# Performance work log

Measured on AMD Instinct MI355X. Metric: run time of the kernel, lower is better.

The kernel has to match this reference:

```python
import jax, jax.numpy as jnp
import numpy as np

B, S, D = 2, 2048, 1024
H, DK, DV = 16, 64, 64


def setup_inputs() -> dict:
    key = jax.random.key(0)
    ks = jax.random.split(key, 12)
    s = 0.02
    return {
        "query": jax.random.normal(ks[0], (B, S, D), jnp.float32),
        "key": jax.random.normal(ks[1], (B, S, D), jnp.float32),
        "value": jax.random.normal(ks[2], (B, S, D), jnp.float32),
        "mask": jax.random.randint(ks[3], (B, S, S), 0, 2, jnp.int32),
        "Wq": jax.random.normal(ks[4], (D, H * DK), jnp.float32) * s,
        "bq": jnp.zeros((H * DK,), jnp.float32),
        "Wk": jax.random.normal(ks[5], (D, H * DK), jnp.float32) * s,
        "bk": jnp.zeros((H * DK,), jnp.float32),
        "Wv": jax.random.normal(ks[6], (D, H * DV), jnp.float32) * s,
        "bv": jnp.zeros((H * DV,), jnp.float32),
        "Wo": jax.random.normal(ks[7], (H * DV, D), jnp.float32) * s,
        "bo": jnp.zeros((D,), jnp.float32),
    }


def reference(query, key, value, mask, Wq, bq, Wk, bk, Wv, bv, Wo, bo):
    temperature = jnp.sqrt(jnp.asarray(DK, query.dtype))
    # projections: [B,S,H*dk] -> [B,H,S,dk]
    q = (query @ Wq + bq).reshape(B, S, H, DK).transpose(0, 2, 1, 3)
    k = (key @ Wk + bk).reshape(B, S, H, DK).transpose(0, 2, 1, 3)
    v = (value @ Wv + bv).reshape(B, S, H, DV).transpose(0, 2, 1, 3)
    # energy: [B,H,Sq,Skv]
    energy = jnp.einsum("bhqd,bhkd->bhqk", q, k) / temperature
    energy = jnp.where(mask[:, None, :, :] == 0, jnp.asarray(-10000.0, energy.dtype), energy)
    attention = jax.nn.softmax(energy, axis=-1)
    attention = jnp.where(jnp.isnan(attention), jnp.asarray(0.0, attention.dtype), attention)
    out = jnp.einsum("bhqk,bhkd->bhqd", attention, v)  # dropout p=0 (eval)
    out = out.transpose(0, 2, 1, 3).reshape(B, S, H * DV)
    out = out @ Wo + bo
    return (out, attention)
```

## Files before the change

### kernel.cpp

```cpp
#include <hip/hip_runtime.h>
#include <stdint.h>


typedef __attribute__((ext_vector_type(8))) __bf16 bf16x8;
typedef __attribute__((ext_vector_type(8))) short short8;
typedef __attribute__((ext_vector_type(4))) float f32x4;

static __device__ __forceinline__ f32x4 mfma_bf16(short8 a, short8 b, f32x4 c) {
  return __builtin_amdgcn_mfma_f32_16x16x32_bf16(
      __builtin_bit_cast(bf16x8, a), __builtin_bit_cast(bf16x8, b), c, 0, 0, 0);
}

static __device__ __forceinline__ unsigned short f2bf(float f) {
  unsigned int u = __float_as_uint(f);
  u += 0x7fffu + ((u >> 16) & 1u);
  return (unsigned short)(u >> 16);
}

static __device__ __forceinline__ void gload_lds16(const void* g, void* l) {
  __builtin_amdgcn_global_load_lds(
      (__attribute__((address_space(1))) void*)(uintptr_t)(g),
      (__attribute__((address_space(3))) void*)(uintptr_t)(l), 16, 0, 0);
}

__global__ __launch_bounds__(256) void conv_f32_bf16(
    const float* q, const float* k, const float* v,
    unsigned short* oq, unsigned short* ok, unsigned short* ov) {
  const float* src = (blockIdx.z == 0) ? q : (blockIdx.z == 1) ? k : v;
  unsigned short* dst = (blockIdx.z == 0) ? oq : (blockIdx.z == 1) ? ok : ov;
  const int i = (blockIdx.x * 256 + threadIdx.x) * 8;
  const float4 a = *(const float4*)&src[i];
  const float4 b = *(const float4*)&src[i + 4];
  unsigned short r[8] = {f2bf(a.x), f2bf(a.y), f2bf(a.z), f2bf(a.w),
                         f2bf(b.x), f2bf(b.y), f2bf(b.z), f2bf(b.w)};
  *(uint4*)&dst[i] = *(uint4*)r;
}

__global__ __launch_bounds__(256) void transpose_w(
    const float* w0, const float* w1, const float* w2, const float* w3,
    unsigned short* o0, unsigned short* o1,
    unsigned short* o2, unsigned short* o3) {
  const float* src = (blockIdx.z == 0) ? w0 : (blockIdx.z == 1) ? w1
                                         : (blockIdx.z == 2) ? w2 : w3;
  unsigned short* dst = (blockIdx.z == 0) ? o0 : (blockIdx.z == 1) ? o1
                                           : (blockIdx.z == 2) ? o2 : o3;
  __shared__ unsigned short tile[64 * 66];
  const int t = threadIdx.x;
  const int r0 = blockIdx.y * 64, c0 = blockIdx.x * 64;
#pragma unroll
  for (int i = 0; i < 4; ++i) {
    const int slot = i * 256 + t;
    const int row = slot >> 4, cg = slot & 15;
    const float4 v = *(const float4*)&src[(r0 + row) * 1024 + c0 + cg * 4];
    unsigned int p0 = (unsigned int)f2bf(v.x) | ((unsigned int)f2bf(v.y) << 16);
    unsigned int p1 = (unsigned int)f2bf(v.z) | ((unsigned int)f2bf(v.w) << 16);
    unsigned int* dp = (unsigned int*)&tile[row * 66 + cg * 4];
    dp[0] = p0;
    dp[1] = p1;
  }
  __syncthreads();
#pragma unroll
  for (int i = 0; i < 2; ++i) {
    const int slot = i * 256 + t;
    const int orow = slot >> 3, kg = slot & 7;
    unsigned short vals[8];
#pragma unroll
    for (int j = 0; j < 8; ++j) vals[j] = tile[(kg * 8 + j) * 66 + orow];
    *(uint4*)&dst[(c0 + orow) * 1024 + r0 + kg * 8] = *(uint4*)vals;
  }
}

__global__ __launch_bounds__(256) void mask_prep(const int* __restrict__ mask,
                                                 unsigned long long* __restrict__ bits) {
  const int wid = (blockIdx.x * 256 + threadIdx.x) >> 6;
  const int lane = threadIdx.x & 63;
  for (int w = wid; w < 131072; w += 2048) {
    const int m = mask[w * 64 + lane];
    const unsigned long long b = __ballot(m != 0);
    if (lane == 0) bits[w] = b;
  }
}

struct GArg {
  const unsigned short* A;
  const unsigned short* BT;
  const float* bias;
  void* C;
  int mode;
};

__global__ __launch_bounds__(256) void gemm_bt(GArg ga, GArg gb, GArg gc) {
  const GArg g = (blockIdx.z == 0) ? ga : (blockIdx.z == 1) ? gb : gc;
  __shared__ alignas(16) unsigned short ash[128 * 64];
  __shared__ alignas(16) unsigned short bsh[128 * 64];
  const int t = threadIdx.x;
  const int wave = t >> 6, lane = t & 63;
  const int m0 = blockIdx.y * 128, n0 = blockIdx.x * 128;
  const int wm = (wave >> 1) * 64, wn = (wave & 1) * 64;
  const int c = lane & 15, gq = lane >> 4;
  const int srow = wave * 8 + (lane >> 3);
  const int scol = (lane & 7) * 8;

  f32x4 zero = {0.f, 0.f, 0.f, 0.f};
  f32x4 acc[4][4];
#pragma unroll
  for (int i = 0; i < 4; ++i)
#pragma unroll
    for (int j = 0; j < 4; ++j) acc[i][j] = zero;

  for (int kk = 0; kk < 16; ++kk) {
    __syncthreads();
    const int kbase = kk * 64;
#pragma unroll
    for (int i = 0; i < 4; ++i) {
      gload_lds16(&g.A[(m0 + i * 32 + srow) * 1024 + kbase + scol],
                  &ash[(i * 32 + wave * 8) * 64]);
      gload_lds16(&g.BT[(n0 + i * 32 + srow) * 1024 + kbase + scol],
                  &bsh[(i * 32 + wave * 8) * 64]);
    }
    __syncthreads();
#pragma unroll
    for (int ks = 0; ks < 2; ++ks) {
      short8 af[4], bf[4];
#pragma unroll
      for (int mt = 0; mt < 4; ++mt)
        af[mt] = *(const short8*)&ash[(wm + mt * 16 + c) * 64 + ks * 32 + gq * 8];
#pragma unroll
      for (int nt = 0; nt < 4; ++nt)
        bf[nt] = *(const short8*)&bsh[(wn + nt * 16 + c) * 64 + ks * 32 + gq * 8];
#pragma unroll
      for (int mt = 0; mt < 4; ++mt)
#pragma unroll
        for (int nt = 0; nt < 4; ++nt)
          acc[mt][nt] = mfma_bf16(af[mt], bf[nt], acc[mt][nt]);
    }
  }
#pragma unroll
  for (int nt = 0; nt < 4; ++nt) {
    const int gcol = n0 + wn + nt * 16 + c;
    const float bia = g.bias[gcol];
#pragma unroll
    for (int mt = 0; mt < 4; ++mt) {
#pragma unroll
      for (int r = 0; r < 4; ++r) {
        const int grow = m0 + wm + mt * 16 + gq * 4 + r;
        const float v = acc[mt][nt][r] + bia;
        if (g.mode == 0) {
          ((unsigned short*)g.C)[grow * 1024 + gcol] = f2bf(v);
        } else if (g.mode == 1) {
          ((unsigned short*)g.C)[((grow >> 11) << 21) + (gcol << 11) + (grow & 2047)] =
              f2bf(v);
        } else {
          ((float*)g.C)[grow * 1024 + gcol] = v;
        }
      }
    }
  }
}

__global__ __launch_bounds__(256) void attn_kern(
    const unsigned short* __restrict__ Qb, const unsigned short* __restrict__ Kb,
    const unsigned short* __restrict__ Vt, const unsigned long long* __restrict__ mbits,
    float* __restrict__ att, unsigned short* __restrict__ Obuf) {
  const int qt = blockIdx.x, h = blockIdx.y, b = blockIdx.z;
  const int t = threadIdx.x, wave = t >> 6, lane = t & 63;
  const int q0 = qt * 64;
  const int c = lane & 15, gq = lane >> 4;
  const int srow = lane >> 3, scol = (lane & 7) * 8;
  const float SCALE = 0.125f * 1.44269504088896341f;

  __shared__ alignas(16) unsigned short qs[64 * 64];
  __shared__ alignas(16) unsigned short kt[64 * 64];
  __shared__ alignas(16) unsigned short vt[64 * 64];
  __shared__ alignas(16) float psf[64 * 64];

#pragma unroll
  for (int i = 0; i < 2; ++i) {
    gload_lds16(&Qb[(b * 2048 + q0 + wave * 16 + i * 8 + srow) * 1024 + h * 64 + scol],
                &qs[(wave * 16 + i * 8) * 64]);
  }

  const unsigned long long* mrow =
      &mbits[(unsigned)(b * 2048 + q0 + wave * 16 + gq * 4) * 32];

  float lsum[4] = {0.f, 0.f, 0.f, 0.f};
  short8 aq[2];
  f32x4 zero = {0.f, 0.f, 0.f, 0.f};

  for (int kv = 0; kv < 32; ++kv) {
    __syncthreads();
#pragma unroll
    for (int i = 0; i < 2; ++i) {
      gload_lds16(&Kb[(b * 2048 + kv * 64 + wave * 16 + i * 8 + srow) * 1024 + h * 64 + scol],
                  &kt[(wave * 16 + i * 8) * 64]);
    }
    __syncthreads();
    if (kv == 0) {
      aq[0] = *(const short8*)&qs[(wave * 16 + c) * 64 + gq * 8];
      aq[1] = *(const short8*)&qs[(wave * 16 + c) * 64 + 32 + gq * 8];
    }
    f32x4 s[4];
#pragma unroll
    for (int nt = 0; nt < 4; ++nt) s[nt] = zero;
#pragma unroll
    for (int ks = 0; ks < 2; ++ks)
#pragma unroll
      for (int nt = 0; nt < 4; ++nt) {
        short8 bk = *(const short8*)&kt[(nt * 16 + c) * 64 + ks * 32 + gq * 8];
        s[nt] = mfma_bf16(aq[ks], bk, s[nt]);
      }
    unsigned long long msh[4];
#pragma unroll
    for (int r = 0; r < 4; ++r) msh[r] = mrow[r * 32 + kv] >> c;
#pragma unroll
    for (int nt = 0; nt < 4; ++nt)
#pragma unroll
      for (int r = 0; r < 4; ++r) {
        const bool on = (msh[r] >> (nt * 16)) & 1ull;
        const float e = on ? s[nt][r] * SCALE : -30.f;
        lsum[r] += __builtin_amdgcn_exp2f(e);
      }
  }
  float linv[4];
#pragma unroll
  for (int r = 0; r < 4; ++r) {
    float v = lsum[r];
    v += __shfl_xor(v, 1);
    v += __shfl_xor(v, 2);
    v += __shfl_xor(v, 4);
    v += __shfl_xor(v, 8);
    linv[r] = 1.0f / v;
  }

  f32x4 o[4];
#pragma unroll
  for (int nt = 0; nt < 4; ++nt) o[nt] = zero;

  for (int kv = 0; kv < 32; ++kv) {
    __syncthreads();
#pragma unroll
    for (int i = 0; i < 2; ++i) {
      gload_lds16(&Kb[(b * 2048 + kv * 64 + wave * 16 + i * 8 + srow) * 1024 + h * 64 + scol],
                  &kt[(wave * 16 + i * 8) * 64]);
      gload_lds16(&Vt[(b << 21) + (h * 64 + wave * 16 + i * 8 + srow) * 2048 + kv * 64 + scol],
                  &vt[(wave * 16 + i * 8) * 64]);
    }
    __syncthreads();
    f32x4 s[4];
#pragma unroll
    for (int nt = 0; nt < 4; ++nt) s[nt] = zero;
#pragma unroll
    for (int ks = 0; ks < 2; ++ks)
#pragma unroll
      for (int nt = 0; nt < 4; ++nt) {
        short8 bk = *(const short8*)&kt[(nt * 16 + c) * 64 + ks * 32 + gq * 8];
        s[nt] = mfma_bf16(aq[ks], bk, s[nt]);
      }
    unsigned long long msh[4];
#pragma unroll
    for (int r = 0; r < 4; ++r) msh[r] = mrow[r * 32 + kv] >> c;
#pragma unroll
    for (int nt = 0; nt < 4; ++nt)
#pragma unroll
      for (int r = 0; r < 4; ++r) {
        const bool on = (msh[r] >> (nt * 16)) & 1ull;
        const float e = on ? s[nt][r] * SCALE : -30.f;
        const float p = __builtin_amdgcn_exp2f(e) * linv[r];
        psf[wave * 1024 + (gq * 4 + r) * 64 + nt * 16 + c] = p;
      }
    __syncthreads();
#pragma unroll
    for (int ks = 0; ks < 2; ++ks) {
      const float4 f0 = *(const float4*)&psf[wave * 1024 + c * 64 + ks * 32 + gq * 8];
      const float4 f1 = *(const float4*)&psf[wave * 1024 + c * 64 + ks * 32 + gq * 8 + 4];
      unsigned short pr[8] = {f2bf(f0.x), f2bf(f0.y), f2bf(f0.z), f2bf(f0.w),
                              f2bf(f1.x), f2bf(f1.y), f2bf(f1.z), f2bf(f1.w)};
      const short8 ap = *(const short8*)pr;
#pragma unroll
      for (int nt = 0; nt < 4; ++nt) {
        short8 bv = *(const short8*)&vt[(nt * 16 + c) * 64 + ks * 32 + gq * 8];
        o[nt] = mfma_bf16(ap, bv, o[nt]);
      }
    }
#pragma unroll
    for (int pass = 0; pass < 4; ++pass) {
      const int row = pass * 4 + (lane >> 4);
      const int col4 = lane & 15;
      const float4 pv = *(const float4*)&psf[wave * 1024 + row * 64 + col4 * 4];
      *(float4*)&att[((long)((b * 16 + h) * 2048 + q0 + wave * 16 + row)) * 2048 +
                     kv * 64 + col4 * 4] = pv;
    }
  }
#pragma unroll
  for (int nt = 0; nt < 4; ++nt)
#pragma unroll
    for (int r = 0; r < 4; ++r) {
      const int row = q0 + wave * 16 + gq * 4 + r;
      Obuf[(b * 2048 + row) * 1024 + h * 64 + nt * 16 + c] = f2bf(o[nt][r]);
    }
}

extern "C" void kernel_launch(void* const* d_in, const int* in_sizes, int n_in,
                              void* d_out, int out_size, void* d_ws, size_t ws_size,
                              hipStream_t stream) {
  const float* query = (const float*)d_in[0];
  const float* key   = (const float*)d_in[1];
  const float* value = (const float*)d_in[2];
  const int* mask    = (const int*)d_in[3];
  const float* Wq = (const float*)d_in[4];
  const float* bq = (const float*)d_in[5];
  const float* Wk = (const float*)d_in[6];
  const float* bk = (const float*)d_in[7];
  const float* Wv = (const float*)d_in[8];
  const float* bv = (const float*)d_in[9];
  const float* Wo = (const float*)d_in[10];
  const float* bo = (const float*)d_in[11];

  float* out = (float*)d_out;
  float* att = out + 4194304;

  char* ws = (char*)d_ws;
  const size_t MB = 1u << 20;
  unsigned short* Aq   = (unsigned short*)(ws);
  unsigned short* Ak   = (unsigned short*)(ws + 8 * MB);
  unsigned short* Av   = (unsigned short*)(ws + 16 * MB);
  unsigned short* Qb   = (unsigned short*)(ws + 24 * MB);
  unsigned short* Kb   = (unsigned short*)(ws + 32 * MB);
  unsigned short* Vt   = (unsigned short*)(ws + 40 * MB);
  unsigned short* Obuf = (unsigned short*)(ws + 48 * MB);
  unsigned short* WqT  = (unsigned short*)(ws + 56 * MB);
  unsigned short* WkT  = (unsigned short*)(ws + 58 * MB);
  unsigned short* WvT  = (unsigned short*)(ws + 60 * MB);
  unsigned short* WoT  = (unsigned short*)(ws + 62 * MB);
  unsigned long long* mbits = (unsigned long long*)(ws + 64 * MB);

  conv_f32_bf16<<<dim3(2048, 1, 3), 256, 0, stream>>>(query, key, value, Aq, Ak, Av);
  transpose_w<<<dim3(16, 16, 4), 256, 0, stream>>>(Wq, Wk, Wv, Wo, WqT, WkT, WvT, WoT);
  mask_prep<<<dim3(512), 256, 0, stream>>>(mask, mbits);

  GArg gq{Aq, WqT, bq, Qb, 0};
  GArg gk{Ak, WkT, bk, Kb, 0};
  GArg gv{Av, WvT, bv, Vt, 1};
  gemm_bt<<<dim3(8, 32, 3), 256, 0, stream>>>(gq, gk, gv);

  attn_kern<<<dim3(32, 16, 2), 256, 0, stream>>>(Qb, Kb, Vt, mbits, att, Obuf);

  GArg go{Obuf, WoT, bo, out, 2};
  gemm_bt<<<dim3(8, 32, 1), 256, 0, stream>>>(go, go, go);
}
```

Measured before the change: 855.7 us.

## Double-buffer K/V tiles with swizzled LDS, precomputed mask nibbles, block remap

Rewrites the two-pass attention kernel to double-buffer the K and V tiles in LDS, prefetching the next tile while the current one is computed. Waits are manual vmcnt/lgkmcnt counts plus raw barriers instead of __syncthreads. It also XOR-swizzles LDS columns to avoid bank conflicts, loads Q directly into registers, and packs mask bits per lane into 64-bit registers once up front instead of reading global memory every iteration. It further remaps block IDs for better L2 locality and raises wave priority around the MFMA sections. In exchange the hand-written waitcnt counts are fragile: the last iteration's vmcnt(4), with stores in flight, could be wrong and cause ordering errors.

```diff
diff --git a/kernel.cpp b/kernel.cpp
--- a/kernel.cpp
+++ b/kernel.cpp
@@ -162,65 +162,119 @@
     const unsigned short* __restrict__ Qb, const unsigned short* __restrict__ Kb,
     const unsigned short* __restrict__ Vt, const unsigned long long* __restrict__ mbits,
     float* __restrict__ att, unsigned short* __restrict__ Obuf) {
-  const int qt = blockIdx.x, h = blockIdx.y, b = blockIdx.z;
+  const int id0 = blockIdx.x + 32 * (blockIdx.y + 16 * blockIdx.z);
+  const int id = (id0 & 7) * 128 + (id0 >> 3);
+  const int qt = id & 31, h = (id >> 5) & 15, b = id >> 9;
   const int t = threadIdx.x, wave = t >> 6, lane = t & 63;
   const int q0 = qt * 64;
   const int c = lane & 15, gq = lane >> 4;
-  const int srow = lane >> 3, scol = (lane & 7) * 8;
+  const int srow = lane >> 3;
+  const int scol_sw = ((lane & 7) ^ srow) * 8;
   const float SCALE = 0.125f * 1.44269504088896341f;
 
-  __shared__ alignas(16) unsigned short qs[64 * 64];
-  __shared__ alignas(16) unsigned short kt[64 * 64];
-  __shared__ alignas(16) unsigned short vt[64 * 64];
-  __shared__ alignas(16) float psf[64 * 64];
-
-#pragma unroll
-  for (int i = 0; i < 2; ++i) {
-    gload_lds16(&Qb[(b * 2048 + q0 + wave * 16 + i * 8 + srow) * 1024 + h * 64 + scol],
-                &qs[(wave * 16 + i * 8) * 64]);
-  }
-
-  const unsigned long long* mrow =
-      &mbits[(unsigned)(b * 2048 + q0 + wave * 16 + gq * 4) * 32];
-
+  __shared__ alignas(16) unsigned short kt[2][64 * 64];
+  __shared__ alignas(16) unsigned short vt[2][64 * 64];
+  __shared__ alignas(16) float psf[4 * 16 * 64];
+
+  auto stage_k = [&](int kvt, int bu) {
+#pragma unroll
+    for (int i = 0; i < 2; ++i)
+      gload_lds16(&Kb[(b * 2048 + kvt * 64 + wave * 16 + i * 8 + srow) * 1024 +
+                      h * 64 + scol_sw],
+                  &kt[bu][(wave * 16 + i * 8) * 64]);
+  };
+  auto stage_v = [&](int kvt, int bu) {
+#pragma unroll
+    for (int i = 0; i < 2; ++i)
+      gload_lds16(&Vt[(b << 21) + (h * 64 + wave * 16 + i * 8 + srow) * 2048 +
+                      kvt * 64 + scol_sw],
+                  &vt[bu][(wave * 16 + i * 8) * 64]);
+  };
+  auto rdcol = [&](int ks) { return (((ks * 4 + gq) ^ (c & 7)) * 8); };
+
+  stage_k(0, 0);
+
+  unsigned long long* msk = (unsigned long long*)psf;
+  {
+    const int row = t >> 2, c8 = (t & 3) * 8;
+    const unsigned long long* src = &mbits[(unsigned)(b * 2048 + q0 + row) * 32 + c8];
+#pragma unroll
+    for (int j = 0; j < 8; ++j) msk[row * 32 + c8 + j] = src[j];
+  }
+  unsigned long long mlo[4], mhi[4];
+#pragma unroll
+  for (int r = 0; r < 4; ++r) {
+    const int row = wave * 16 + gq * 4 + r;
+    unsigned long long lo = 0, hi = 0;
+#pragma unroll
+    for (int kvi = 0; kvi < 16; ++kvi) {
+      const unsigned long long w0 = msk[row * 32 + kvi] >> c;
+      const unsigned long long w1 = msk[row * 32 + 16 + kvi] >> c;
+      const unsigned long long n0 =
+          (w0 & 1) | ((w0 >> 15) & 2) | ((w0 >> 30) & 4) | ((w0 >> 45) & 8);
+      const unsigned long long n1 =
+          (w1 & 1) | ((w1 >> 15) & 2) | ((w1 >> 30) & 4) | ((w1 >> 45) & 8);
+      lo |= n0 << (kvi * 4);
+      hi |= n1 << (kvi * 4);
+    }
+    mlo[r] = lo;
+    mhi[r] = hi;
+  }
+
+  short8 aq[2];
+  {
+    const unsigned short* qrow = &Qb[(b * 2048 + q0 + wave * 16 + c) * 1024 + h * 64];
+    aq[0] = *(const short8*)&qrow[gq * 8];
+    aq[1] = *(const short8*)&qrow[32 + gq * 8];
+  }
+
+  asm volatile("s_waitcnt vmcnt(0) lgkmcnt(0)" ::: "memory");
+  __builtin_amdgcn_s_barrier();
+  __builtin_amdgcn_sched_barrier(0);
+
+  const f32x4 zero = {0.f, 0.f, 0.f, 0.f};
   float lsum[4] = {0.f, 0.f, 0.f, 0.f};
-  short8 aq[2];
-  f32x4 zero = {0.f, 0.f, 0.f, 0.f};
-
+  int buf = 0;
+
+#pragma unroll 1
   for (int kv = 0; kv < 32; ++kv) {
-    __syncthreads();
-#pragma unroll
-    for (int i = 0; i < 2; ++i) {
-      gload_lds16(&Kb[(b * 2048 + kv * 64 + wave * 16 + i * 8 + srow) * 1024 + h * 64 + scol],
-                  &kt[(wave * 16 + i * 8) * 64]);
-    }
-    __syncthreads();
-    if (kv == 0) {
-      aq[0] = *(const short8*)&qs[(wave * 16 + c) * 64 + gq * 8];
-      aq[1] = *(const short8*)&qs[(wave * 16 + c) * 64 + 32 + gq * 8];
-    }
+    if (kv < 31) {
+      stage_k(kv + 1, buf ^ 1);
+      asm volatile("s_waitcnt vmcnt(2)" ::: "memory");
+    } else {
+      asm volatile("s_waitcnt vmcnt(0)" ::: "memory");
+    }
+    __builtin_amdgcn_s_barrier();
+    __builtin_amdgcn_sched_barrier(0);
+
     f32x4 s[4];
 #pragma unroll
     for (int nt = 0; nt < 4; ++nt) s[nt] = zero;
+    __builtin_amdgcn_s_setprio(1);
 #pragma unroll
     for (int ks = 0; ks < 2; ++ks)
 #pragma unroll
       for (int nt = 0; nt < 4; ++nt) {
-        short8 bk = *(const short8*)&kt[(nt * 16 + c) * 64 + ks * 32 + gq * 8];
+        const short8 bk = *(const short8*)&kt[buf][(nt * 16 + c) * 64 + rdcol(ks)];
         s[nt] = mfma_bf16(aq[ks], bk, s[nt]);
       }
-    unsigned long long msh[4];
-#pragma unroll
-    for (int r = 0; r < 4; ++r) msh[r] = mrow[r * 32 + kv] >> c;
-#pragma unroll
-    for (int nt = 0; nt < 4; ++nt)
-#pragma unroll
-      for (int r = 0; r < 4; ++r) {
-        const bool on = (msh[r] >> (nt * 16)) & 1ull;
-        const float e = on ? s[nt][r] * SCALE : -30.f;
+    __builtin_amdgcn_s_setprio(0);
+#pragma unroll
+    for (int r = 0; r < 4; ++r) {
+      const unsigned long long mr = (kv < 16) ? mlo[r] : mhi[r];
+      const unsigned nib = (unsigned)(mr >> ((kv & 15) * 4)) & 0xFu;
+#pragma unroll
+      for (int nt = 0; nt < 4; ++nt) {
+        const float e = ((nib >> nt) & 1u) ? s[nt][r] * SCALE : -30.f;
         lsum[r] += __builtin_amdgcn_exp2f(e);
       }
-  }
+    }
+    asm volatile("s_waitcnt lgkmcnt(0)" ::: "memory");
+    __builtin_amdgcn_s_barrier();
+    __builtin_amdgcn_sched_barrier(0);
+    buf ^= 1;
+  }
+
   float linv[4];
 #pragma unroll
   for (int r = 0; r < 4; ++r) {
@@ -236,39 +290,47 @@
 #pragma unroll
   for (int nt = 0; nt < 4; ++nt) o[nt] = zero;
 
+  stage_k(0, buf);
+  stage_v(0, buf);
+  asm volatile("s_waitcnt vmcnt(0)" ::: "memory");
+  __builtin_amdgcn_s_barrier();
+  __builtin_amdgcn_sched_barrier(0);
+
+#pragma unroll 1
   for (int kv = 0; kv < 32; ++kv) {
-    __syncthreads();
-#pragma unroll
-    for (int i = 0; i < 2; ++i) {
-      gload_lds16(&Kb[(b * 2048 + kv * 64 + wave * 16 + i * 8 + srow) * 1024 + h * 64 + scol],
-                  &kt[(wave * 16 + i * 8) * 64]);
-      gload_lds16(&Vt[(b << 21) + (h * 64 + wave * 16 + i * 8 + srow) * 2048 + kv * 64 + scol],
-                  &vt[(wave * 16 + i * 8) * 64]);
-    }
-    __syncthreads();
+    if (kv < 31) {
+      stage_k(kv + 1, buf ^ 1);
+      stage_v(kv + 1, buf ^ 1);
+      asm volatile("s_waitcnt vmcnt(4)" ::: "memory");
+    } else {
+      asm volatile("s_waitcnt vmcnt(4)" ::: "memory");
+    }
+    __builtin_amdgcn_s_barrier();
+    __builtin_amdgcn_sched_barrier(0);
+
     f32x4 s[4];
 #pragma unroll
     for (int nt = 0; nt < 4; ++nt) s[nt] = zero;
+    __builtin_amdgcn_s_setprio(1);
 #pragma unroll
     for (int ks = 0; ks < 2; ++ks)
 #pragma unroll
       for (int nt = 0; nt < 4; ++nt) {
-        short8 bk = *(const short8*)&kt[(nt * 16 + c) * 64 + ks * 32 + gq * 8];
+        const short8 bk = *(const short8*)&kt[buf][(nt * 16 + c) * 64 + rdcol(ks)];
         s[nt] = mfma_bf16(aq[ks], bk, s[nt]);
       }
-    unsigned long long msh[4];
-#pragma unroll
-    for (int r = 0; r < 4; ++r) msh[r] = mrow[r * 32 + kv] >> c;
-#pragma unroll
-    for (int nt = 0; nt < 4; ++nt)
-#pragma unroll
-      for (int r = 0; r < 4; ++r) {
-        const bool on = (msh[r] >> (nt * 16)) & 1ull;
-        const float e = on ? s[nt][r] * SCALE : -30.f;
+    __builtin_amdgcn_s_setprio(0);
+#pragma unroll
+    for (int r = 0; r < 4; ++r) {
+      const unsigned long long mr = (kv < 16) ? mlo[r] : mhi[r];
+      const unsigned nib = (unsigned)(mr >> ((kv & 15) * 4)) & 0xFu;
+#pragma unroll
+      for (int nt = 0; nt < 4; ++nt) {
+        const float e = ((nib >> nt) & 1u) ? s[nt][r] * SCALE : -30.f;
         const float p = __builtin_amdgcn_exp2f(e) * linv[r];
         psf[wave * 1024 + (gq * 4 + r) * 64 + nt * 16 + c] = p;
       }
-    __syncthreads();
+    }
 #pragma unroll
     for (int ks = 0; ks < 2; ++ks) {
       const float4 f0 = *(const float4*)&psf[wave * 1024 + c * 64 + ks * 32 + gq * 8];
@@ -276,11 +338,13 @@
       unsigned short pr[8] = {f2bf(f0.x), f2bf(f0.y), f2bf(f0.z), f2bf(f0.w),
                               f2bf(f1.x), f2bf(f1.y), f2bf(f1.z), f2bf(f1.w)};
       const short8 ap = *(const short8*)pr;
+      __builtin_amdgcn_s_setprio(1);
 #pragma unroll
       for (int nt = 0; nt < 4; ++nt) {
-        short8 bv = *(const short8*)&vt[(nt * 16 + c) * 64 + ks * 32 + gq * 8];
+        const short8 bv = *(const short8*)&vt[buf][(nt * 16 + c) * 64 + rdcol(ks)];
         o[nt] = mfma_bf16(ap, bv, o[nt]);
       }
+      __builtin_amdgcn_s_setprio(0);
     }
 #pragma unroll
     for (int pass = 0; pass < 4; ++pass) {
@@ -290,7 +354,12 @@
       *(float4*)&att[((long)((b * 16 + h) * 2048 + q0 + wave * 16 + row)) * 2048 +
                      kv * 64 + col4 * 4] = pv;
     }
-  }
+    asm volatile("s_waitcnt lgkmcnt(0)" ::: "memory");
+    __builtin_amdgcn_s_barrier();
+    __builtin_amdgcn_sched_barrier(0);
+    buf ^= 1;
+  }
+
 #pragma unroll
   for (int nt = 0; nt < 4; ++nt)
 #pragma unroll
```

Measured after the change: 837.2 us. 1.02x faster.
